# Optimization experiments

Measured on AMD Instinct MI355X. Metric: run time of the kernel, lower is better.

Reference implementation:

```python
import jax, jax.numpy as jnp
import numpy as np

DIM = 1024
N_HEADS = 16

def setup_inputs() -> dict:
    key = jax.random.key(0)
    ks = jax.random.split(key, 6)
    s = 1.0 / np.sqrt(DIM)
    return {
        "x": jax.random.normal(ks[0], (2, 2048, DIM), dtype=jnp.float32),
        "Wq": jax.random.normal(ks[1], (DIM, DIM), dtype=jnp.float32) * s,
        "Wk": jax.random.normal(ks[2], (DIM, DIM), dtype=jnp.float32) * s,
        "Wv": jax.random.normal(ks[3], (DIM, DIM), dtype=jnp.float32) * s,
        "Wo": jax.random.normal(ks[4], (DIM, DIM), dtype=jnp.float32) * s,
        "bo": jax.random.normal(ks[5], (DIM,), dtype=jnp.float32) * 0.01,
    }

def reference(x, Wq, Wk, Wv, Wo, bo):
    B, S, D = x.shape
    H = N_HEADS
    hd = D // H
    # linear layers: y = x @ W.T (torch convention)
    def proj(W):
        y = jnp.einsum('bsd,ed->bse', x, W)
        return y.reshape(B, S, H, hd).transpose(0, 2, 1, 3)  # [B,H,S,hd]
    q, k, v = proj(Wq), proj(Wk), proj(Wv)
    attn = jnp.einsum('bhqd,bhkd->bhqk', q, k) / jnp.sqrt(jnp.float32(hd))
    attn = jax.nn.softmax(attn, axis=-1)
    out = jnp.einsum('bhqk,bhkd->bhqd', attn, v)
    out = out.transpose(0, 2, 1, 3).reshape(B, S, D)
    out = jnp.einsum('bsd,ed->bse', out, Wo) + bo
    return out
```

## Files before the change

### kernel.cpp

```cpp
#include <hip/hip_runtime.h>
#include <hip/hip_bf16.h>

#define SEQ 2048
#define DIM 1024
#define NH 16
#define HD 64
#define MTOT 4096

typedef __attribute__((ext_vector_type(8))) short bf16x8;
typedef __attribute__((ext_vector_type(4))) float f32x4;
typedef __attribute__((ext_vector_type(16))) float f32x16;
typedef __attribute__((ext_vector_type(4))) unsigned int u32x4;
typedef __attribute__((ext_vector_type(2))) unsigned int u32x2;

typedef const __attribute__((address_space(1))) void* gptr_t;
typedef __attribute__((address_space(3))) void* sptr_t;

static __device__ __forceinline__ unsigned short f2bf(float f) {
    unsigned int u = __builtin_bit_cast(unsigned int, f);
    return (unsigned short)((u + 0x7FFFu + ((u >> 16) & 1u)) >> 16);
}

#define CVTPK(d, x, y) asm("v_cvt_pk_bf16_f32 %0, %1, %2" : "=v"(d) : "v"(x), "v"(y))
#define PLSWAP(a, b) asm("v_permlane32_swap_b32 %0, %1" : "+v"(a), "+v"(b))

__global__ void cast_kernel(const float* __restrict__ in, unsigned short* __restrict__ out, int n) {
    int i = (blockIdx.x * 256 + threadIdx.x) * 4;
    if (i < n) {
        float4 v = *reinterpret_cast<const float4*>(in + i);
        ushort4 o;
        o.x = f2bf(v.x); o.y = f2bf(v.y); o.z = f2bf(v.z); o.w = f2bf(v.w);
        *reinterpret_cast<ushort4*>(out + i) = o;
    }
}

template<int MODE>
__global__ __launch_bounds__(256) void gemm_nt(
    const unsigned short* __restrict__ A,
    const unsigned short* __restrict__ B0,
    const unsigned short* __restrict__ B1,
    const unsigned short* __restrict__ B2,
    unsigned short* __restrict__ D0,
    unsigned short* __restrict__ D1,
    unsigned short* __restrict__ D2,
    float* __restrict__ Df,
    const float* __restrict__ bias)
{
    constexpr int K = DIM;
    __shared__ __align__(16) unsigned short Asm[128 * 32];
    __shared__ __align__(16) unsigned short Bsm[128 * 32];

    const int tid = threadIdx.x;
    const int wave = tid >> 6, lane = tid & 63;
    const int wm = wave >> 1, wn = wave & 1;
    const int m0 = blockIdx.y * 128, n0 = blockIdx.x * 128;
    const int fr = lane & 15;

    const unsigned short* Bsel = (MODE == 1 || blockIdx.z == 0) ? B0 : (blockIdx.z == 1 ? B1 : B2);

    const int srow = wave * 32 + (lane >> 2);
    const int schunk = (lane & 3) ^ ((lane >> 3) & 3);
    const size_t abase = (size_t)(m0 + srow) * K + (size_t)schunk * 8;
    const size_t bbase = (size_t)(n0 + srow) * K + (size_t)schunk * 8;

    f32x4 acc[4][4] = {};

    for (int k0 = 0; k0 < K; k0 += 32) {
        #pragma unroll
        for (int c = 0; c < 2; ++c) {
            __builtin_amdgcn_global_load_lds(
                (gptr_t)(A + abase + (size_t)c * 16 * K + k0),
                (sptr_t)((char*)Asm + wave * 2048 + c * 1024), 16, 0, 0);
            __builtin_amdgcn_global_load_lds(
                (gptr_t)(Bsel + bbase + (size_t)c * 16 * K + k0),
                (sptr_t)((char*)Bsm + wave * 2048 + c * 1024), 16, 0, 0);
        }
        __syncthreads();

        bf16x8 af[4], bf[4];
        const int ca = ((lane >> 4) ^ ((fr >> 1) & 3)) * 16;
        #pragma unroll
        for (int i = 0; i < 4; ++i) {
            int ra = wm * 64 + i * 16 + fr;
            int rb = wn * 64 + i * 16 + fr;
            af[i] = *(const bf16x8*)((const char*)Asm + ra * 64 + ca);
            bf[i] = *(const bf16x8*)((const char*)Bsm + rb * 64 + ca);
        }
        #pragma unroll
        for (int i = 0; i < 4; ++i)
            #pragma unroll
            for (int j = 0; j < 4; ++j)
                acc[i][j] = __builtin_amdgcn_mfma_f32_16x16x32_bf16(af[i], bf[j], acc[i][j], 0, 0, 0);
        __syncthreads();
    }

    if (MODE == 0) {
        unsigned short* Dst = (blockIdx.z == 0) ? D0 : (blockIdx.z == 1 ? D1 : D2);
        const float scale = (blockIdx.z == 0) ? 0.1803368787f : 1.0f;
        #pragma unroll
        for (int i = 0; i < 4; ++i)
            #pragma unroll
            for (int j = 0; j < 4; ++j)
                #pragma unroll
                for (int r = 0; r < 4; ++r) {
                    int m = m0 + wm * 64 + i * 16 + (lane >> 4) * 4 + r;
                    int n = n0 + wn * 64 + j * 16 + fr;
                    int b = m >> 11, s = m & 2047, h = n >> 6, dh = n & 63;
                    Dst[(((size_t)(b * NH + h)) * SEQ + s) * HD + dh] = f2bf(acc[i][j][r] * scale);
                }
    } else {
        #pragma unroll
        for (int i = 0; i < 4; ++i)
            #pragma unroll
            for (int j = 0; j < 4; ++j)
                #pragma unroll
                for (int r = 0; r < 4; ++r) {
                    int m = m0 + wm * 64 + i * 16 + (lane >> 4) * 4 + r;
                    int n = n0 + wn * 64 + j * 16 + fr;
                    Df[(size_t)m * DIM + n] = acc[i][j][r] + bias[n];
                }
    }
}

__global__ __launch_bounds__(512, 2) void attn_kernel(
    const unsigned short* __restrict__ Q,
    const unsigned short* __restrict__ Kg,
    const unsigned short* __restrict__ Vg,
    unsigned short* __restrict__ O)
{
    __shared__ __align__(16) unsigned short Ksm[2][64 * 66];
    __shared__ __align__(16) unsigned short Vsm[2][64 * 66];

    const int tid = threadIdx.x;
    const int wave = tid >> 6, lane = tid & 63;
    const int lq = lane & 31, hi = lane >> 5;

    const int bid = blockIdx.x;
    const int xcd = bid & 7, slot = bid >> 3;
    const int bh = xcd * 4 + (slot & 3);
    const int q0 = (slot >> 2) * 256;

    const unsigned short* Qh = Q + (size_t)bh * SEQ * HD;
    const unsigned short* Kh = Kg + (size_t)bh * SEQ * HD;
    const unsigned short* Vh = Vg + (size_t)bh * SEQ * HD;

    const float MCONST = 12.0f;

    const int qrow = q0 + wave * 32 + lq;
    bf16x8 qf[4];
    #pragma unroll
    for (int dch = 0; dch < 4; ++dch)
        qf[dch] = *(const bf16x8*)(Qh + (size_t)qrow * HD + dch * 16 + hi * 8);

    f32x16 ot0 = {}, ot1 = {};
    float l = 0.f;

    const int krow_s = tid >> 3, kch_s = tid & 7;
    const int kvp_s = tid >> 4, sub_s = tid & 1;
    const int dch_s = (tid >> 1) & 7;

    bf16x8 sk, sv;
    auto stage_load = [&](int t64) {
        sk = *(const bf16x8*)(Kh + (size_t)(t64 + krow_s) * HD + kch_s * 8);
        sv = *(const bf16x8*)(Vh + (size_t)(t64 + 2 * kvp_s + sub_s) * HD + dch_s * 8);
    };
    auto stage_write = [&](int buf) {
        u32x4 kw = __builtin_bit_cast(u32x4, sk);
        unsigned* kp = (unsigned*)((char*)&Ksm[buf][0] + 132 * krow_s + 16 * kch_s);
        kp[0] = kw[0]; kp[1] = kw[1]; kp[2] = kw[2]; kp[3] = kw[3];
        u32x4 vw = __builtin_bit_cast(u32x4, sv);
        unsigned p0 = (unsigned)__shfl_xor((int)vw[0], 1);
        unsigned p1 = (unsigned)__shfl_xor((int)vw[1], 1);
        unsigned p2 = (unsigned)__shfl_xor((int)vw[2], 1);
        unsigned p3 = (unsigned)__shfl_xor((int)vw[3], 1);
        unsigned ea0 = sub_s ? p2 : vw[0];
        unsigned ea1 = sub_s ? p3 : vw[1];
        unsigned eb0 = sub_s ? vw[2] : p0;
        unsigned eb1 = sub_s ? vw[3] : p1;
        unsigned* vp = (unsigned*)&Vsm[buf][0];
        const int dbase = dch_s * 8 + sub_s * 4;
        vp[33 * (dbase + 0) + kvp_s] = (ea0 & 0xffffu) | (eb0 << 16);
        vp[33 * (dbase + 1) + kvp_s] = (ea0 >> 16) | (eb0 & 0xffff0000u);
        vp[33 * (dbase + 2) + kvp_s] = (ea1 & 0xffffu) | (eb1 << 16);
        vp[33 * (dbase + 3) + kvp_s] = (ea1 >> 16) | (eb1 & 0xffff0000u);
    };

    stage_load(0);
    stage_write(0);
    __syncthreads();

    int cur = 0;
    #pragma unroll 1
    for (int t = 0; t < SEQ / 64; ++t) {
        if (t + 1 < SEQ / 64) stage_load((t + 1) * 64);

        const char* Kb = (const char*)&Ksm[cur][0];
        const char* Vb = (const char*)&Vsm[cur][0];

        f32x16 st0, st1;
        #pragma unroll
        for (int r = 0; r < 16; ++r) { st0[r] = -MCONST; st1[r] = -MCONST; }
        __builtin_amdgcn_s_setprio(1);
        #pragma unroll
        for (int dch = 0; dch < 4; ++dch) {
            const unsigned* a0 = (const unsigned*)(Kb + 132 * lq + 32 * dch + 16 * hi);
            const unsigned* a1 = (const unsigned*)(Kb + 132 * (32 + lq) + 32 * dch + 16 * hi);
            u32x4 f0 = {a0[0], a0[1], a0[2], a0[3]};
            u32x4 f1 = {a1[0], a1[1], a1[2], a1[3]};
            st0 = __builtin_amdgcn_mfma_f32_32x32x16_bf16(__builtin_bit_cast(bf16x8, f0), qf[dch], st0, 0, 0, 0);
            st1 = __builtin_amdgcn_mfma_f32_32x32x16_bf16(__builtin_bit_cast(bf16x8, f1), qf[dch], st1, 0, 0, 0);
        }
        __builtin_amdgcn_s_setprio(0);

        float sa = 0.f, sb = 0.f, sc = 0.f, sd = 0.f;
        #pragma unroll
        for (int r = 0; r < 16; r += 4) {
            st0[r]     = exp2f(st0[r]);     sa += st0[r];
            st0[r + 1] = exp2f(st0[r + 1]); sb += st0[r + 1];
            st0[r + 2] = exp2f(st0[r + 2]); sc += st0[r + 2];
            st0[r + 3] = exp2f(st0[r + 3]); sd += st0[r + 3];
        }
        #pragma unroll
        for (int r = 0; r < 16; r += 4) {
            st1[r]     = exp2f(st1[r]);     sa += st1[r];
            st1[r + 1] = exp2f(st1[r + 1]); sb += st1[r + 1];
            st1[r + 2] = exp2f(st1[r + 2]); sc += st1[r + 2];
            st1[r + 3] = exp2f(st1[r + 3]); sd += st1[r + 3];
        }
        float ps = (sa + sb) + (sc + sd);
        ps += __shfl_xor(ps, 32);
        l += ps;

        bf16x8 pf0, pf1, pf2, pf3;
        {
            unsigned w0, w1, w2, w3, w4, w5, w6, w7;
            CVTPK(w0, st0[0], st0[1]);   CVTPK(w1, st0[2], st0[3]);
            CVTPK(w2, st0[4], st0[5]);   CVTPK(w3, st0[6], st0[7]);
            CVTPK(w4, st0[8], st0[9]);   CVTPK(w5, st0[10], st0[11]);
            CVTPK(w6, st0[12], st0[13]); CVTPK(w7, st0[14], st0[15]);
            PLSWAP(w0, w2); PLSWAP(w1, w3); PLSWAP(w4, w6); PLSWAP(w5, w7);
            u32x4 uA = {w0, w1, w2, w3}, uB = {w4, w5, w6, w7};
            pf0 = __builtin_bit_cast(bf16x8, uA);
            pf1 = __builtin_bit_cast(bf16x8, uB);
        }
        {
            unsigned w0, w1, w2, w3, w4, w5, w6, w7;
            CVTPK(w0, st1[0], st1[1]);   CVTPK(w1, st1[2], st1[3]);
            CVTPK(w2, st1[4], st1[5]);   CVTPK(w3, st1[6], st1[7]);
            CVTPK(w4, st1[8], st1[9]);   CVTPK(w5, st1[10], st1[11]);
            CVTPK(w6, st1[12], st1[13]); CVTPK(w7, st1[14], st1[15]);
            PLSWAP(w0, w2); PLSWAP(w1, w3); PLSWAP(w4, w6); PLSWAP(w5, w7);
            u32x4 uA = {w0, w1, w2, w3}, uB = {w4, w5, w6, w7};
            pf2 = __builtin_bit_cast(bf16x8, uA);
            pf3 = __builtin_bit_cast(bf16x8, uB);
        }

        __builtin_amdgcn_s_setprio(1);
        #pragma unroll
        for (int kc = 0; kc < 4; ++kc) {
            const unsigned* v0 = (const unsigned*)(Vb + 132 * lq + 32 * kc + 16 * hi);
            const unsigned* v1 = (const unsigned*)(Vb + 132 * (32 + lq) + 32 * kc + 16 * hi);
            u32x4 g0 = {v0[0], v0[1], v0[2], v0[3]};
            u32x4 g1 = {v1[0], v1[1], v1[2], v1[3]};
            bf16x8 pfv = (kc == 0) ? pf0 : (kc == 1) ? pf1 : (kc == 2) ? pf2 : pf3;
            ot0 = __builtin_amdgcn_mfma_f32_32x32x16_bf16(__builtin_bit_cast(bf16x8, g0), pfv, ot0, 0, 0, 0);
            ot1 = __builtin_amdgcn_mfma_f32_32x32x16_bf16(__builtin_bit_cast(bf16x8, g1), pfv, ot1, 0, 0, 0);
        }
        __builtin_amdgcn_s_setprio(0);

        if (t + 1 < SEQ / 64) stage_write(cur ^ 1);
        __syncthreads();
        cur ^= 1;
    }

    const float inv = 1.0f / l;
    const int b = bh >> 4, h = bh & 15;
    unsigned short* orow = O + ((size_t)(b * SEQ + qrow)) * DIM + h * HD;
    #pragma unroll
    for (int tg = 0; tg < 4; ++tg) {
        unsigned wA, wB;
        CVTPK(wA, ot0[4 * tg + 0] * inv, ot0[4 * tg + 1] * inv);
        CVTPK(wB, ot0[4 * tg + 2] * inv, ot0[4 * tg + 3] * inv);
        u32x2 wlo = {wA, wB};
        *(u32x2*)(orow + 8 * tg + 4 * hi) = wlo;
        CVTPK(wA, ot1[4 * tg + 0] * inv, ot1[4 * tg + 1] * inv);
        CVTPK(wB, ot1[4 * tg + 2] * inv, ot1[4 * tg + 3] * inv);
        u32x2 whi = {wA, wB};
        *(u32x2*)(orow + 32 + 8 * tg + 4 * hi) = whi;
    }
}

extern "C" void kernel_launch(void* const* d_in, const int* in_sizes, int n_in,
                              void* d_out, int out_size, void* d_ws, size_t ws_size,
                              hipStream_t stream) {
    const float* x  = (const float*)d_in[0];
    const float* Wq = (const float*)d_in[1];
    const float* Wk = (const float*)d_in[2];
    const float* Wv = (const float*)d_in[3];
    const float* Wo = (const float*)d_in[4];
    const float* bo = (const float*)d_in[5];
    float* out = (float*)d_out;

    unsigned short* ws = (unsigned short*)d_ws;
    unsigned short* xb  = ws;
    unsigned short* wqb = xb + (size_t)MTOT * DIM;
    unsigned short* wkb = wqb + (size_t)DIM * DIM;
    unsigned short* wvb = wkb + (size_t)DIM * DIM;
    unsigned short* wob = wvb + (size_t)DIM * DIM;
    unsigned short* qb  = wob + (size_t)DIM * DIM;
    unsigned short* kb  = qb + (size_t)MTOT * DIM;
    unsigned short* vb  = kb + (size_t)MTOT * DIM;
    unsigned short* ob  = vb + (size_t)MTOT * DIM;

    cast_kernel<<<dim3(MTOT * DIM / 1024), 256, 0, stream>>>(x, xb, MTOT * DIM);
    cast_kernel<<<dim3(DIM * DIM / 1024), 256, 0, stream>>>(Wq, wqb, DIM * DIM);
    cast_kernel<<<dim3(DIM * DIM / 1024), 256, 0, stream>>>(Wk, wkb, DIM * DIM);
    cast_kernel<<<dim3(DIM * DIM / 1024), 256, 0, stream>>>(Wv, wvb, DIM * DIM);
    cast_kernel<<<dim3(DIM * DIM / 1024), 256, 0, stream>>>(Wo, wob, DIM * DIM);

    gemm_nt<0><<<dim3(DIM / 128, MTOT / 128, 3), 256, 0, stream>>>(
        xb, wqb, wkb, wvb, qb, kb, vb, nullptr, nullptr);

    attn_kernel<<<dim3(256), 512, 0, stream>>>(qb, kb, vb, ob);

    gemm_nt<1><<<dim3(DIM / 128, MTOT / 128, 1), 256, 0, stream>>>(
        ob, wob, nullptr, nullptr, nullptr, nullptr, nullptr, out, bo);
}
```

Before: 134.6 us.

## Split attention KV range in two halves and merge partials in separate kernel

The attention kernel now splits each query tile's key/value sequence into two halves processed by separate blocks, doubling the grid from 256 to 512 blocks so more CUs are busy. Each block writes unnormalized fp32 partial outputs and row sums to workspace, and a new merge kernel adds the two halves, normalizes and converts to bf16. Merging with a plain sum works only because the softmax uses a fixed max constant. The change adds a kernel launch and extra fp32 global traffic for the partials. The launch-bounds occupancy hint is also raised to 4 blocks per CU.

```diff
diff --git a/kernel.cpp b/kernel.cpp
--- a/kernel.cpp
+++ b/kernel.cpp
@@ -122,11 +122,12 @@
     }
 }
 
-__global__ __launch_bounds__(512, 2) void attn_kernel(
+__global__ __launch_bounds__(512, 4) void attn_kernel(
     const unsigned short* __restrict__ Q,
     const unsigned short* __restrict__ Kg,
     const unsigned short* __restrict__ Vg,
-    unsigned short* __restrict__ O)
+    float* __restrict__ po,
+    float* __restrict__ ml)
 {
     __shared__ __align__(16) unsigned short Ksm[2][64 * 66];
     __shared__ __align__(16) unsigned short Vsm[2][64 * 66];
@@ -138,7 +139,10 @@
     const int bid = blockIdx.x;
     const int xcd = bid & 7, slot = bid >> 3;
     const int bh = xcd * 4 + (slot & 3);
-    const int q0 = (slot >> 2) * 256;
+    const int rest = slot >> 2;
+    const int q0 = (rest >> 1) * 256;
+    const int half = rest & 1;
+    const int kvbase = half * 1024;
 
     const unsigned short* Qh = Q + (size_t)bh * SEQ * HD;
     const unsigned short* Kh = Kg + (size_t)bh * SEQ * HD;
@@ -185,14 +189,14 @@
         vp[33 * (dbase + 3) + kvp_s] = (ea1 >> 16) | (eb1 & 0xffff0000u);
     };
 
-    stage_load(0);
+    stage_load(kvbase);
     stage_write(0);
     __syncthreads();
 
     int cur = 0;
     #pragma unroll 1
-    for (int t = 0; t < SEQ / 64; ++t) {
-        if (t + 1 < SEQ / 64) stage_load((t + 1) * 64);
+    for (int t = 0; t < 16; ++t) {
+        if (t < 15) stage_load(kvbase + (t + 1) * 64);
 
         const char* Kb = (const char*)&Ksm[cur][0];
         const char* Vb = (const char*)&Vsm[cur][0];
@@ -268,26 +272,48 @@
         }
         __builtin_amdgcn_s_setprio(0);
 
-        if (t + 1 < SEQ / 64) stage_write(cur ^ 1);
+        if (t < 15) stage_write(cur ^ 1);
         __syncthreads();
         cur ^= 1;
     }
 
-    const float inv = 1.0f / l;
-    const int b = bh >> 4, h = bh & 15;
-    unsigned short* orow = O + ((size_t)(b * SEQ + qrow)) * DIM + h * HD;
+    const size_t prow = (size_t)(half * 32 + bh) * SEQ + qrow;
+    float* por = po + prow * 64;
     #pragma unroll
     for (int tg = 0; tg < 4; ++tg) {
-        unsigned wA, wB;
-        CVTPK(wA, ot0[4 * tg + 0] * inv, ot0[4 * tg + 1] * inv);
-        CVTPK(wB, ot0[4 * tg + 2] * inv, ot0[4 * tg + 3] * inv);
-        u32x2 wlo = {wA, wB};
-        *(u32x2*)(orow + 8 * tg + 4 * hi) = wlo;
-        CVTPK(wA, ot1[4 * tg + 0] * inv, ot1[4 * tg + 1] * inv);
-        CVTPK(wB, ot1[4 * tg + 2] * inv, ot1[4 * tg + 3] * inv);
-        u32x2 whi = {wA, wB};
-        *(u32x2*)(orow + 32 + 8 * tg + 4 * hi) = whi;
-    }
+        f32x4 v0 = {ot0[4 * tg + 0], ot0[4 * tg + 1], ot0[4 * tg + 2], ot0[4 * tg + 3]};
+        *(f32x4*)(por + 8 * tg + 4 * hi) = v0;
+        f32x4 v1 = {ot1[4 * tg + 0], ot1[4 * tg + 1], ot1[4 * tg + 2], ot1[4 * tg + 3]};
+        *(f32x4*)(por + 32 + 8 * tg + 4 * hi) = v1;
+    }
+    if (hi == 0) ml[prow] = l;
+}
+
+__global__ __launch_bounds__(256) void merge_kernel(
+    const float* __restrict__ po,
+    const float* __restrict__ ml,
+    unsigned short* __restrict__ ob)
+{
+    const int gid = blockIdx.x * 256 + threadIdx.x;
+    const int row = gid >> 3, dch = gid & 7;
+    const size_t p1 = row, p2 = (size_t)32 * SEQ + row;
+    const float inv = 1.0f / (ml[p1] + ml[p2]);
+
+    f32x4 a0 = *(const f32x4*)(po + p1 * 64 + dch * 8);
+    f32x4 a1 = *(const f32x4*)(po + p1 * 64 + dch * 8 + 4);
+    f32x4 b0 = *(const f32x4*)(po + p2 * 64 + dch * 8);
+    f32x4 b1 = *(const f32x4*)(po + p2 * 64 + dch * 8 + 4);
+
+    unsigned wA, wB, wC, wD;
+    CVTPK(wA, (a0[0] + b0[0]) * inv, (a0[1] + b0[1]) * inv);
+    CVTPK(wB, (a0[2] + b0[2]) * inv, (a0[3] + b0[3]) * inv);
+    CVTPK(wC, (a1[0] + b1[0]) * inv, (a1[1] + b1[1]) * inv);
+    CVTPK(wD, (a1[2] + b1[2]) * inv, (a1[3] + b1[3]) * inv);
+    u32x4 w = {wA, wB, wC, wD};
+
+    const int bh = row >> 11, s = row & 2047;
+    const int b = bh >> 4, h = bh & 15;
+    *(u32x4*)(ob + ((size_t)(b * SEQ + s)) * DIM + h * HD + dch * 8) = w;
 }
 
 extern "C" void kernel_launch(void* const* d_in, const int* in_sizes, int n_in,
@@ -311,6 +337,8 @@
     unsigned short* kb  = qb + (size_t)MTOT * DIM;
     unsigned short* vb  = kb + (size_t)MTOT * DIM;
     unsigned short* ob  = vb + (size_t)MTOT * DIM;
+    float* po = (float*)(ob + (size_t)MTOT * DIM);
+    float* ml = po + (size_t)2 * 32 * SEQ * 64;
 
     cast_kernel<<<dim3(MTOT * DIM / 1024), 256, 0, stream>>>(x, xb, MTOT * DIM);
     cast_kernel<<<dim3(DIM * DIM / 1024), 256, 0, stream>>>(Wq, wqb, DIM * DIM);
@@ -321,7 +349,9 @@
     gemm_nt<0><<<dim3(DIM / 128, MTOT / 128, 3), 256, 0, stream>>>(
         xb, wqb, wkb, wvb, qb, kb, vb, nullptr, nullptr);
 
-    attn_kernel<<<dim3(256), 512, 0, stream>>>(qb, kb, vb, ob);
+    attn_kernel<<<dim3(512), 512, 0, stream>>>(qb, kb, vb, po, ml);
+
+    merge_kernel<<<dim3(2048), 256, 0, stream>>>(po, ml, ob);
 
     gemm_nt<1><<<dim3(DIM / 128, MTOT / 128, 1), 256, 0, stream>>>(
         ob, wob, nullptr, nullptr, nullptr, nullptr, nullptr, out, bo);
```

Measured after the change: 144.8 us. 1.08x slower.

## Store V pre-transposed in tiles from QKV GEMM and swizzle attention LDS

Applied to the files above, without the earlier changes.

The QKV projection epilogue now writes V in a per-64-key-tile transposed layout ([bh][tile][dh][key]) using packed bf16 stores. The attention kernel can then stage K and V into LDS with plain 16-byte stores instead of shuffle-based in-kernel transposition. Bank conflicts are avoided with an XOR swizzle rather than row padding, so fragments load as single 128-bit LDS reads. This cuts VALU and LDS work in the attention inner loop, at the cost of more scattered 8-byte global stores in the GEMM epilogue.

```diff
diff --git a/kernel.cpp b/kernel.cpp
--- a/kernel.cpp
+++ b/kernel.cpp
@@ -95,19 +95,37 @@
     }
 
     if (MODE == 0) {
-        unsigned short* Dst = (blockIdx.z == 0) ? D0 : (blockIdx.z == 1 ? D1 : D2);
-        const float scale = (blockIdx.z == 0) ? 0.1803368787f : 1.0f;
-        #pragma unroll
-        for (int i = 0; i < 4; ++i)
+        if (blockIdx.z == 2) {
             #pragma unroll
-            for (int j = 0; j < 4; ++j)
+            for (int i = 0; i < 4; ++i)
                 #pragma unroll
-                for (int r = 0; r < 4; ++r) {
-                    int m = m0 + wm * 64 + i * 16 + (lane >> 4) * 4 + r;
+                for (int j = 0; j < 4; ++j) {
                     int n = n0 + wn * 64 + j * 16 + fr;
-                    int b = m >> 11, s = m & 2047, h = n >> 6, dh = n & 63;
-                    Dst[(((size_t)(b * NH + h)) * SEQ + s) * HD + dh] = f2bf(acc[i][j][r] * scale);
+                    int h = n >> 6, dh = n & 63;
+                    int mb = m0 + wm * 64 + i * 16 + (lane >> 4) * 4;
+                    int b = mb >> 11, s = mb & 2047;
+                    int t = s >> 6, kin = s & 63;
+                    unsigned wA, wB;
+                    CVTPK(wA, acc[i][j][0], acc[i][j][1]);
+                    CVTPK(wB, acc[i][j][2], acc[i][j][3]);
+                    u32x2 w = {wA, wB};
+                    *(u32x2*)(D2 + ((((size_t)(b * NH + h) * 32 + t) * 64 + dh) << 6) + kin) = w;
                 }
+        } else {
+            unsigned short* Dst = (blockIdx.z == 0) ? D0 : D1;
+            const float scale = (blockIdx.z == 0) ? 0.1803368787f : 1.0f;
+            #pragma unroll
+            for (int i = 0; i < 4; ++i)
+                #pragma unroll
+                for (int j = 0; j < 4; ++j)
+                    #pragma unroll
+                    for (int r = 0; r < 4; ++r) {
+                        int m = m0 + wm * 64 + i * 16 + (lane >> 4) * 4 + r;
+                        int n = n0 + wn * 64 + j * 16 + fr;
+                        int b = m >> 11, s = m & 2047, h = n >> 6, dh = n & 63;
+                        Dst[(((size_t)(b * NH + h)) * SEQ + s) * HD + dh] = f2bf(acc[i][j][r] * scale);
+                    }
+        }
     } else {
         #pragma unroll
         for (int i = 0; i < 4; ++i)
@@ -125,11 +143,11 @@
 __global__ __launch_bounds__(512, 2) void attn_kernel(
     const unsigned short* __restrict__ Q,
     const unsigned short* __restrict__ Kg,
-    const unsigned short* __restrict__ Vg,
+    const unsigned short* __restrict__ Vt,
     unsigned short* __restrict__ O)
 {
-    __shared__ __align__(16) unsigned short Ksm[2][64 * 66];
-    __shared__ __align__(16) unsigned short Vsm[2][64 * 66];
+    __shared__ __align__(16) unsigned short Ksm[2][64 * 64];
+    __shared__ __align__(16) unsigned short Vsm[2][64 * 64];
 
     const int tid = threadIdx.x;
     const int wave = tid >> 6, lane = tid & 63;
@@ -142,7 +160,7 @@
 
     const unsigned short* Qh = Q + (size_t)bh * SEQ * HD;
     const unsigned short* Kh = Kg + (size_t)bh * SEQ * HD;
-    const unsigned short* Vh = Vg + (size_t)bh * SEQ * HD;
+    const unsigned short* Vh = Vt + (size_t)bh * SEQ * HD;
 
     const float MCONST = 12.0f;
 
@@ -155,39 +173,24 @@
     f32x16 ot0 = {}, ot1 = {};
     float l = 0.f;
 
-    const int krow_s = tid >> 3, kch_s = tid & 7;
-    const int kvp_s = tid >> 4, sub_s = tid & 1;
-    const int dch_s = (tid >> 1) & 7;
+    const int srow = tid >> 3, sch = tid & 7;
+    const int swoff = 128 * srow + 16 * (sch ^ (srow & 7));
 
     bf16x8 sk, sv;
     auto stage_load = [&](int t64) {
-        sk = *(const bf16x8*)(Kh + (size_t)(t64 + krow_s) * HD + kch_s * 8);
-        sv = *(const bf16x8*)(Vh + (size_t)(t64 + 2 * kvp_s + sub_s) * HD + dch_s * 8);
+        sk = *(const bf16x8*)(Kh + (size_t)(t64 + srow) * HD + sch * 8);
+        sv = *(const bf16x8*)(Vh + (size_t)t64 * 64 + srow * 64 + sch * 8);
     };
     auto stage_write = [&](int buf) {
-        u32x4 kw = __builtin_bit_cast(u32x4, sk);
-        unsigned* kp = (unsigned*)((char*)&Ksm[buf][0] + 132 * krow_s + 16 * kch_s);
-        kp[0] = kw[0]; kp[1] = kw[1]; kp[2] = kw[2]; kp[3] = kw[3];
-        u32x4 vw = __builtin_bit_cast(u32x4, sv);
-        unsigned p0 = (unsigned)__shfl_xor((int)vw[0], 1);
-        unsigned p1 = (unsigned)__shfl_xor((int)vw[1], 1);
-        unsigned p2 = (unsigned)__shfl_xor((int)vw[2], 1);
-        unsigned p3 = (unsigned)__shfl_xor((int)vw[3], 1);
-        unsigned ea0 = sub_s ? p2 : vw[0];
-        unsigned ea1 = sub_s ? p3 : vw[1];
-        unsigned eb0 = sub_s ? vw[2] : p0;
-        unsigned eb1 = sub_s ? vw[3] : p1;
-        unsigned* vp = (unsigned*)&Vsm[buf][0];
-        const int dbase = dch_s * 8 + sub_s * 4;
-        vp[33 * (dbase + 0) + kvp_s] = (ea0 & 0xffffu) | (eb0 << 16);
-        vp[33 * (dbase + 1) + kvp_s] = (ea0 >> 16) | (eb0 & 0xffff0000u);
-        vp[33 * (dbase + 2) + kvp_s] = (ea1 & 0xffffu) | (eb1 << 16);
-        vp[33 * (dbase + 3) + kvp_s] = (ea1 >> 16) | (eb1 & 0xffff0000u);
+        *(bf16x8*)((char*)&Ksm[buf][0] + swoff) = sk;
+        *(bf16x8*)((char*)&Vsm[buf][0] + swoff) = sv;
     };
 
     stage_load(0);
     stage_write(0);
     __syncthreads();
+
+    const int x7 = lq & 7;
 
     int cur = 0;
     #pragma unroll 1
@@ -203,12 +206,10 @@
         __builtin_amdgcn_s_setprio(1);
         #pragma unroll
         for (int dch = 0; dch < 4; ++dch) {
-            const unsigned* a0 = (const unsigned*)(Kb + 132 * lq + 32 * dch + 16 * hi);
-            const unsigned* a1 = (const unsigned*)(Kb + 132 * (32 + lq) + 32 * dch + 16 * hi);
-            u32x4 f0 = {a0[0], a0[1], a0[2], a0[3]};
-            u32x4 f1 = {a1[0], a1[1], a1[2], a1[3]};
-            st0 = __builtin_amdgcn_mfma_f32_32x32x16_bf16(__builtin_bit_cast(bf16x8, f0), qf[dch], st0, 0, 0, 0);
-            st1 = __builtin_amdgcn_mfma_f32_32x32x16_bf16(__builtin_bit_cast(bf16x8, f1), qf[dch], st1, 0, 0, 0);
+            bf16x8 kf0 = *(const bf16x8*)(Kb + 128 * lq + 16 * ((2 * dch + hi) ^ x7));
+            bf16x8 kf1 = *(const bf16x8*)(Kb + 128 * (32 + lq) + 16 * ((2 * dch + hi) ^ x7));
+            st0 = __builtin_amdgcn_mfma_f32_32x32x16_bf16(kf0, qf[dch], st0, 0, 0, 0);
+            st1 = __builtin_amdgcn_mfma_f32_32x32x16_bf16(kf1, qf[dch], st1, 0, 0, 0);
         }
         __builtin_amdgcn_s_setprio(0);
 
@@ -258,13 +259,11 @@
         __builtin_amdgcn_s_setprio(1);
         #pragma unroll
         for (int kc = 0; kc < 4; ++kc) {
-            const unsigned* v0 = (const unsigned*)(Vb + 132 * lq + 32 * kc + 16 * hi);
-            const unsigned* v1 = (const unsigned*)(Vb + 132 * (32 + lq) + 32 * kc + 16 * hi);
-            u32x4 g0 = {v0[0], v0[1], v0[2], v0[3]};
-            u32x4 g1 = {v1[0], v1[1], v1[2], v1[3]};
+            bf16x8 vf0 = *(const bf16x8*)(Vb + 128 * lq + 16 * ((2 * kc + hi) ^ x7));
+            bf16x8 vf1 = *(const bf16x8*)(Vb + 128 * (32 + lq) + 16 * ((2 * kc + hi) ^ x7));
             bf16x8 pfv = (kc == 0) ? pf0 : (kc == 1) ? pf1 : (kc == 2) ? pf2 : pf3;
-            ot0 = __builtin_amdgcn_mfma_f32_32x32x16_bf16(__builtin_bit_cast(bf16x8, g0), pfv, ot0, 0, 0, 0);
-            ot1 = __builtin_amdgcn_mfma_f32_32x32x16_bf16(__builtin_bit_cast(bf16x8, g1), pfv, ot1, 0, 0, 0);
+            ot0 = __builtin_amdgcn_mfma_f32_32x32x16_bf16(vf0, pfv, ot0, 0, 0, 0);
+            ot1 = __builtin_amdgcn_mfma_f32_32x32x16_bf16(vf1, pfv, ot1, 0, 0, 0);
         }
         __builtin_amdgcn_s_setprio(0);
 
@@ -309,8 +308,8 @@
     unsigned short* wob = wvb + (size_t)DIM * DIM;
     unsigned short* qb  = wob + (size_t)DIM * DIM;
     unsigned short* kb  = qb + (size_t)MTOT * DIM;
-    unsigned short* vb  = kb + (size_t)MTOT * DIM;
-    unsigned short* ob  = vb + (size_t)MTOT * DIM;
+    unsigned short* vtb = kb + (size_t)MTOT * DIM;
+    unsigned short* ob  = vtb + (size_t)MTOT * DIM;
 
     cast_kernel<<<dim3(MTOT * DIM / 1024), 256, 0, stream>>>(x, xb, MTOT * DIM);
     cast_kernel<<<dim3(DIM * DIM / 1024), 256, 0, stream>>>(Wq, wqb, DIM * DIM);
@@ -319,9 +318,9 @@
     cast_kernel<<<dim3(DIM * DIM / 1024), 256, 0, stream>>>(Wo, wob, DIM * DIM);
 
     gemm_nt<0><<<dim3(DIM / 128, MTOT / 128, 3), 256, 0, stream>>>(
-        xb, wqb, wkb, wvb, qb, kb, vb, nullptr, nullptr);
-
-    attn_kernel<<<dim3(256), 512, 0, stream>>>(qb, kb, vb, ob);
+        xb, wqb, wkb, wvb, qb, kb, vtb, nullptr, nullptr);
+
+    attn_kernel<<<dim3(256), 512, 0, stream>>>(qb, kb, vtb, ob);
 
     gemm_nt<1><<<dim3(DIM / 128, MTOT / 128, 1), 256, 0, stream>>>(
         ob, wob, nullptr, nullptr, nullptr, nullptr, nullptr, out, bo);
```

After: 154.0 us. +14.4%, slower.
